# Performance work log

Measured on AMD Instinct MI355X. Metric: run time of the kernel, lower is better.

The kernel has to match this reference:

```python
import jax, jax.numpy as jnp
import numpy as np

N_NODES = 100000
N_EDGES = 6400000
HID = 32


def setup_inputs() -> dict:
    key = jax.random.key(0)
    ks = jax.random.split(key, 24)
    inp = {
        "x_G": jax.random.normal(ks[0], (N_NODES, 1), dtype=jnp.float32),
        "edge_index_G": jax.random.randint(ks[1], (2, N_EDGES), 0, N_NODES, dtype=jnp.int32),
        "x_H": jax.random.normal(ks[2], (N_NODES, 1), dtype=jnp.float32),
        "edge_index_H": jax.random.randint(ks[3], (2, N_EDGES), 0, N_NODES, dtype=jnp.int32),
    }
    ki = 4
    for i in range(3):
        d_in = 1 if i == 0 else HID
        inp[f"W1_{i}"] = jax.random.normal(ks[ki], (d_in, HID), dtype=jnp.float32) / np.sqrt(d_in); ki += 1
        inp[f"b1_{i}"] = jnp.zeros((HID,), dtype=jnp.float32)
        inp[f"W2_{i}"] = jax.random.normal(ks[ki], (HID, HID), dtype=jnp.float32) / np.sqrt(HID); ki += 1
        inp[f"b2_{i}"] = jnp.zeros((HID,), dtype=jnp.float32)
    inp["Wc1"] = jax.random.normal(ks[ki], (2 * HID, HID), dtype=jnp.float32) / np.sqrt(2 * HID); ki += 1
    inp["bc1"] = jnp.zeros((HID,), dtype=jnp.float32)
    inp["Wc2"] = jax.random.normal(ks[ki], (HID, 1), dtype=jnp.float32) / np.sqrt(HID); ki += 1
    inp["bc2"] = jnp.zeros((1,), dtype=jnp.float32)
    return inp


def _encode(x, edge_index, layers):
    n = x.shape[0]
    src, dst = edge_index[0], edge_index[1]
    for (W1, b1, W2, b2) in layers:
        # GIN aggregation: sum of neighbor messages scattered to targets; eps = 0
        agg = jax.ops.segment_sum(x[src], dst, num_segments=n)  # [N, d]
        h = x + agg  # (1 + eps) * x + agg with eps = 0
        h = jax.nn.relu(h @ W1 + b1) @ W2 + b2  # GIN MLP
        x = jax.nn.relu(h)  # outer F.relu in encode loop
    return jnp.sum(x, axis=0, keepdims=True)  # global_add_pool, single graph -> [1, HID]


def reference(x_G, edge_index_G, x_H, edge_index_H,
              W1_0, b1_0, W2_0, b2_0,
              W1_1, b1_1, W2_1, b2_1,
              W1_2, b1_2, W2_2, b2_2,
              Wc1, bc1, Wc2, bc2):
    layers = [(W1_0, b1_0, W2_0, b2_0),
              (W1_1, b1_1, W2_1, b2_1),
              (W1_2, b1_2, W2_2, b2_2)]
    h_G = _encode(x_G, edge_index_G, layers)
    h_H = _encode(x_H, edge_index_H, layers)
    combined = jnp.concatenate([h_G, h_H], axis=1)  # [1, 2*HID]
    out = jax.nn.relu(combined @ Wc1 + bc1) @ Wc2 + bc2
    return jax.nn.sigmoid(out)
```

## Files before the change

### kernel.cpp

```cpp
#include <hip/hip_runtime.h>
#include <hip/hip_bf16.h>
#include <math.h>
#include <string.h>

#define HID 32
#define PSHIFT 8
#define NPB (1 << PSHIFT)
#define MAXP 512
#define SLOTS 17408
#define SBITS 3
#define SBINS (1 << SBITS)
#define NBINS (NPB * SBINS)
#define GS 32
#define HS_ROWS 32
#define COLBUF 3072
#define COLBUF0 6144
typedef unsigned short u16;
typedef unsigned char u8;
typedef float f32x2 __attribute__((ext_vector_type(2)));

__device__ inline float e42f_sw(unsigned b) {
    unsigned u = (b & 0x7fu) << 20;
    float f; memcpy(&f, &u, 4);
    return f * 0x1p120f;
}
__device__ inline unsigned f2e4_sw(float f) {
    f = fminf(f, 448.f);
    float y = f * 0x1p-120f;
    unsigned r; memcpy(&r, &y, 4);
    r = r + 0x7FFFFu + ((r >> 20) & 1u);
    return (r >> 20) & 0x7fu;
}
__device__ inline void acc_e4(float* a, unsigned w) {
#if __has_builtin(__builtin_amdgcn_cvt_pk_f32_fp8)
    f32x2 lo = __builtin_amdgcn_cvt_pk_f32_fp8(w, false);
    f32x2 hi = __builtin_amdgcn_cvt_pk_f32_fp8(w, true);
    a[0] += lo.x; a[1] += lo.y; a[2] += hi.x; a[3] += hi.y;
#else
    a[0] += e42f_sw(w);
    a[1] += e42f_sw(w >> 8);
    a[2] += e42f_sw(w >> 16);
    a[3] += e42f_sw(w >> 24);
#endif
}
__device__ inline unsigned pack_e4(float o0, float o1, float o2, float o3) {
#if __has_builtin(__builtin_amdgcn_cvt_pk_fp8_f32)
    unsigned pw = (unsigned)__builtin_amdgcn_cvt_pk_fp8_f32(
        fminf(o0, 448.f), fminf(o1, 448.f), 0, false);
    pw = (unsigned)__builtin_amdgcn_cvt_pk_fp8_f32(
        fminf(o2, 448.f), fminf(o3, 448.f), pw, true);
    return pw;
#else
    return f2e4_sw(o0) | (f2e4_sw(o1) << 8) | (f2e4_sw(o2) << 16) | (f2e4_sw(o3) << 24);
#endif
}

__global__ void zero_kernel(float* __restrict__ p, int n) {
    int i = blockIdx.x * blockDim.x + threadIdx.x;
    if (i < n) p[i] = 0.f;
}
__global__ void init_gcur(int* __restrict__ gcur, int P) {
    int b = blockIdx.x * blockDim.x + threadIdx.x;
    if (b < P) gcur[b * GS] = b * SLOTS;
}

__global__ void partition_edges(const int* __restrict__ src, const int* __restrict__ dst,
                                int* __restrict__ gcur, unsigned* __restrict__ staged,
                                int E, int P) {
    __shared__ int h[4][MAXP];
    __shared__ int hbase[MAXP];
    __shared__ int cur[MAXP];
    __shared__ int gbase[MAXP];
    __shared__ unsigned sortedv[4096];
    __shared__ u16 bktid[4096];
    __shared__ int wsums[4];
    __shared__ int sTotal;
    int t = threadIdx.x, wid = t >> 6, lane = t & 63;
    for (int i = t; i < 4 * MAXP; i += 256) (&h[0][0])[i] = 0;
    __syncthreads();

    int base = blockIdx.x * 4096;
    int4 S[4], D[4];
#pragma unroll
    for (int r = 0; r < 4; r++) {
        int e = base + r * 1024 + t * 4;
        if (e + 3 < E) {
            S[r] = *(const int4*)(src + e);
            D[r] = *(const int4*)(dst + e);
        } else {
            int s0[4], d0[4];
            for (int j = 0; j < 4; j++) {
                int ee = e + j;
                s0[j] = (ee < E) ? src[ee] : -1;
                d0[j] = (ee < E) ? dst[ee] : -1;
            }
            S[r] = make_int4(s0[0], s0[1], s0[2], s0[3]);
            D[r] = make_int4(d0[0], d0[1], d0[2], d0[3]);
        }
        if (D[r].x >= 0) atomicAdd(&h[wid][D[r].x >> PSHIFT], 1);
        if (D[r].y >= 0) atomicAdd(&h[wid][D[r].y >> PSHIFT], 1);
        if (D[r].z >= 0) atomicAdd(&h[wid][D[r].z >> PSHIFT], 1);
        if (D[r].w >= 0) atomicAdd(&h[wid][D[r].w >> PSHIFT], 1);
    }
    __syncthreads();

    int b0 = 2 * t, b1 = 2 * t + 1;
    int t0 = (b0 < P) ? (h[0][b0] + h[1][b0] + h[2][b0] + h[3][b0]) : 0;
    int t1 = (b1 < P) ? (h[0][b1] + h[1][b1] + h[2][b1] + h[3][b1]) : 0;
    int s = t0 + t1;
    int incl = s;
#pragma unroll
    for (int off = 1; off < 64; off <<= 1) {
        int u = __shfl_up(incl, off, 64);
        if (lane >= off) incl += u;
    }
    if (lane == 63) wsums[wid] = incl;
    __syncthreads();
    int woff = 0;
#pragma unroll
    for (int w = 0; w < 4; w++) if (w < wid) woff += wsums[w];
    int excl = woff + incl - s;
    if (b0 < P) { hbase[b0] = excl;      cur[b0] = excl; }
    if (b1 < P) { hbase[b1] = excl + t0; cur[b1] = excl + t0; }
    if (b0 < P && t0) gbase[b0] = atomicAdd(&gcur[b0 * GS], t0);
    if (b1 < P && t1) gbase[b1] = atomicAdd(&gcur[b1 * GS], t1);
    if (t == 255) sTotal = excl + s;
    __syncthreads();

#pragma unroll
    for (int r = 0; r < 4; r++) {
        int ss[4] = { S[r].x, S[r].y, S[r].z, S[r].w };
        int dd[4] = { D[r].x, D[r].y, D[r].z, D[r].w };
#pragma unroll
        for (int j = 0; j < 4; j++) {
            int d = dd[j];
            if (d >= 0) {
                int bk = d >> PSHIFT;
                int pos = atomicAdd(&cur[bk], 1);
                sortedv[pos] = ((unsigned)(d & (NPB - 1)) << 17) | (unsigned)ss[j];
                bktid[pos]   = (u16)bk;
            }
        }
    }
    __syncthreads();

    int total = sTotal;
    for (int i = t; i < total; i += 256) {
        int bk = bktid[i];
        int addr = gbase[bk] + (i - hbase[bk]);
        if (addr < (bk + 1) * SLOTS)
            staged[addr] = sortedv[i];
    }
}

__global__ void scan_buckets(const int* __restrict__ gcur, int* __restrict__ colbase,
                             int* __restrict__ rowptr, int P, int N) {
    __shared__ int wsums[4];
    int t = threadIdx.x, wid = t >> 6, lane = t & 63;
    int b0 = 2 * t, b1 = 2 * t + 1;
    int c0 = 0, c1 = 0;
    if (b0 < P) { c0 = gcur[b0 * GS] - b0 * SLOTS; if (c0 > SLOTS) c0 = SLOTS; }
    if (b1 < P) { c1 = gcur[b1 * GS] - b1 * SLOTS; if (c1 > SLOTS) c1 = SLOTS; }
    int s = c0 + c1;
    int incl = s;
#pragma unroll
    for (int off = 1; off < 64; off <<= 1) {
        int u = __shfl_up(incl, off, 64);
        if (lane >= off) incl += u;
    }
    if (lane == 63) wsums[wid] = incl;
    __syncthreads();
    int woff = 0;
#pragma unroll
    for (int w = 0; w < 4; w++) if (w < wid) woff += wsums[w];
    int excl = woff + incl - s;
    if (b0 < P) colbase[b0] = excl;
    if (b1 < P) colbase[b1] = excl + c0;
    if (t == 255) {
        colbase[P] = excl + s;
        rowptr[N]  = excl + s;
    }
}

__global__ void sort_bucket(const unsigned* __restrict__ staged, const int* __restrict__ gcur,
                            const int* __restrict__ colbase,
                            int* __restrict__ rowptr, int* __restrict__ col, int N) {
    __shared__ int cnt[NBINS];
    __shared__ int wsum[4];
    __shared__ int sorted[SLOTS];
    int b = blockIdx.x;
    int t = threadIdx.x;
    int lane = t & 63, wid = t >> 6;
    int sBeg = b * SLOTS;
    int sEnd = gcur[b * GS]; if (sEnd > sBeg + SLOTS) sEnd = sBeg + SLOTS;
    int total = sEnd - sBeg;
    int colStart = colbase[b];
    int nodeBase = b << PSHIFT;

    for (int i = t; i < NBINS; i += 256) cnt[i] = 0;
    __syncthreads();
    for (int i = sBeg + t; i < sEnd; i += 256) {
        unsigned w = staged[i];
        int key = (int)((w >> 17) << SBITS) | (int)((w & 0x1FFFFu) >> 14);
        atomicAdd(&cnt[key], 1);
    }
    __syncthreads();

    int loc[SBINS]; int tot = 0;
#pragma unroll
    for (int k = 0; k < SBINS; k++) { loc[k] = tot; tot += cnt[(t << SBITS) + k]; }
    int incl = tot;
#pragma unroll
    for (int off = 1; off < 64; off <<= 1) {
        int u = __shfl_up(incl, off, 64);
        if (lane >= off) incl += u;
    }
    if (lane == 63) wsum[wid] = incl;
    __syncthreads();
    int woff = 0;
#pragma unroll
    for (int w = 0; w < 4; w++) if (w < wid) woff += wsum[w];
    int excl = woff + incl - tot;
    int node = nodeBase + t;
    if (node < N) rowptr[node] = colStart + excl;
#pragma unroll
    for (int k = 0; k < SBINS; k++) cnt[(t << SBITS) + k] = excl + loc[k];
    __syncthreads();

    for (int i = sBeg + t; i < sEnd; i += 256) {
        unsigned w = staged[i];
        int key = (int)((w >> 17) << SBITS) | (int)((w & 0x1FFFFu) >> 14);
        int pos = atomicAdd(&cnt[key], 1);
        sorted[pos] = (int)(w & 0x1FFFFu);
    }
    __syncthreads();
    for (int i = t; i < total; i += 256)
        col[colStart + i] = sorted[i];
}

__global__ void mlp0_fused(const int* __restrict__ rowptr, const int* __restrict__ col,
                           const float* __restrict__ x0,
                           const float* __restrict__ W1, const float* __restrict__ b1,
                           const float* __restrict__ W2, const float* __restrict__ b2,
                           u8* __restrict__ out, int n) {
    __shared__ float sW1[HID], sb1[HID], sW2[HID * HID], sb2[HID];
    __shared__ int colbuf[COLBUF0];
    int t = threadIdx.x;
    if (t < HID) { sW1[t] = W1[t]; sb1[t] = b1[t]; sb2[t] = b2[t]; }
    for (int i = t; i < HID * HID; i += blockDim.x) sW2[i] = W2[i];

    int firstNode = blockIdx.x * 64;
    int lastNode  = firstNode + 64; if (lastNode > n) lastNode = n;
    int blockStart = (firstNode < n) ? rowptr[firstNode] : 0;
    int blockEnd   = (firstNode < n) ? rowptr[lastNode] : 0;
    int stagedCnt = blockEnd - blockStart; if (stagedCnt > COLBUF0) stagedCnt = COLBUF0;
    for (int i = t; i < stagedCnt; i += 256) colbuf[i] = col[blockStart + i];
    __syncthreads();

    int node = firstNode + (t >> 2);
    int q    = t & 3;
    int lane = t & 63;
    int base = lane & ~3;
    bool active = node < n;

    float s = 0.f;
    if (active) {
        int beg = rowptr[node], end = rowptr[node + 1];
        int jSplit = blockStart + stagedCnt; if (jSplit > end) jSplit = end;
        int j = beg + q;
        for (; j + 12 < jSplit; j += 16) {
            int c0 = colbuf[j - blockStart];
            int c1 = colbuf[j + 4 - blockStart];
            int c2 = colbuf[j + 8 - blockStart];
            int c3 = colbuf[j + 12 - blockStart];
            s += x0[c0]; s += x0[c1]; s += x0[c2]; s += x0[c3];
        }
        for (; j < jSplit; j += 4) s += x0[colbuf[j - blockStart]];
        for (; j < end; j += 4) s += x0[col[j]];
    }
    s += __shfl_xor(s, 1, 64);
    s += __shfl_xor(s, 2, 64);
    float v = active ? (x0[node] + s) : 0.f;

    float h[8];
#pragma unroll
    for (int i = 0; i < 8; i++) h[i] = fmaxf(fmaf(v, sW1[q * 8 + i], sb1[q * 8 + i]), 0.f);
    float o[8];
#pragma unroll
    for (int i = 0; i < 8; i++) o[i] = sb2[q * 8 + i];
#pragma unroll
    for (int k = 0; k < HID; k++) {
        float hk = __shfl(h[k & 7], base | (k >> 3), 64);
#pragma unroll
        for (int i = 0; i < 8; i++) o[i] = fmaf(hk, sW2[k * HID + q * 8 + i], o[i]);
    }
    if (active) {
        unsigned w0 = pack_e4(fmaxf(o[0], 0.f), fmaxf(o[1], 0.f),
                              fmaxf(o[2], 0.f), fmaxf(o[3], 0.f));
        unsigned w1 = pack_e4(fmaxf(o[4], 0.f), fmaxf(o[5], 0.f),
                              fmaxf(o[6], 0.f), fmaxf(o[7], 0.f));
        uint2 pk = make_uint2(w0, w1);
        *(uint2*)(out + ((size_t)node << 5) + (q << 3)) = pk;
    }
}

template <bool REDUCE>
__global__ void mlp_fused(const int* __restrict__ rowptr, const int* __restrict__ col,
                          const u8* __restrict__ xin,
                          const float* __restrict__ W1, const float* __restrict__ b1,
                          const float* __restrict__ W2, const float* __restrict__ b2,
                          u8* __restrict__ xout, float* __restrict__ hsum, int n) {
    __shared__ float sW1[HID * HID], sb1[HID], sW2[HID * HID], sb2[HID];
    __shared__ int colbuf[COLBUF];
    __shared__ float red[4][HID];
    int t = threadIdx.x;
    for (int i = t; i < HID * HID; i += blockDim.x) { sW1[i] = W1[i]; sW2[i] = W2[i]; }
    if (t < HID) { sb1[t] = b1[t]; sb2[t] = b2[t]; }

    int firstNode = blockIdx.x * 32;
    int lastNode  = firstNode + 32; if (lastNode > n) lastNode = n;
    int blockStart = (firstNode < n) ? rowptr[firstNode] : 0;
    int blockEnd   = (firstNode < n) ? rowptr[lastNode] : 0;
    int stagedCnt = blockEnd - blockStart; if (stagedCnt > COLBUF) stagedCnt = COLBUF;
    for (int i = t; i < stagedCnt; i += 256) colbuf[i] = col[blockStart + i];
    __syncthreads();

    int node = firstNode + (t >> 3);
    int q    = t & 7;
    int lane = t & 63;
    int base = lane & ~7;
    bool active = node < n;

    float va[4];
#pragma unroll
    for (int i = 0; i < 4; i++) va[i] = 0.f;
    if (active) {
        int beg = rowptr[node], end = rowptr[node + 1];
        const u8* xq = xin + (q << 2);
        float a0[4], a1[4], a2[4], a3[4];
#pragma unroll
        for (int i = 0; i < 4; i++) a0[i] = a1[i] = a2[i] = a3[i] = 0.f;
        {
            unsigned w = *(const unsigned*)(xq + ((size_t)node << 5));
            acc_e4(a0, w);
        }
        int jSplit = blockStart + stagedCnt; if (jSplit > end) jSplit = end;
        int j = beg;
        for (; j + 8 <= jSplit; j += 8) {
            int lj = j - blockStart;
            int c0 = colbuf[lj+0], c1 = colbuf[lj+1], c2 = colbuf[lj+2], c3 = colbuf[lj+3];
            int c4 = colbuf[lj+4], c5 = colbuf[lj+5], c6 = colbuf[lj+6], c7 = colbuf[lj+7];
            unsigned w0 = *(const unsigned*)(xq + ((size_t)c0 << 5));
            unsigned w1 = *(const unsigned*)(xq + ((size_t)c1 << 5));
            unsigned w2 = *(const unsigned*)(xq + ((size_t)c2 << 5));
            unsigned w3 = *(const unsigned*)(xq + ((size_t)c3 << 5));
            unsigned w4 = *(const unsigned*)(xq + ((size_t)c4 << 5));
            unsigned w5 = *(const unsigned*)(xq + ((size_t)c5 << 5));
            unsigned w6 = *(const unsigned*)(xq + ((size_t)c6 << 5));
            unsigned w7 = *(const unsigned*)(xq + ((size_t)c7 << 5));
            acc_e4(a0, w0); acc_e4(a1, w1); acc_e4(a2, w2); acc_e4(a3, w3);
            acc_e4(a0, w4); acc_e4(a1, w5); acc_e4(a2, w6); acc_e4(a3, w7);
        }
        for (; j < jSplit; j++) {
            unsigned w = *(const unsigned*)(xq + ((size_t)colbuf[j - blockStart] << 5));
            acc_e4(a0, w);
        }
        for (; j < end; j++) {
            unsigned w = *(const unsigned*)(xq + ((size_t)col[j] << 5));
            acc_e4(a0, w);
        }
#pragma unroll
        for (int i = 0; i < 4; i++) va[i] = (a0[i] + a1[i]) + (a2[i] + a3[i]);
    }

    float h[4];
#pragma unroll
    for (int i = 0; i < 4; i++) h[i] = sb1[q * 4 + i];
#pragma unroll
    for (int k = 0; k < HID; k++) {
        float vk = __shfl(va[k & 3], base | (k >> 2), 64);
#pragma unroll
        for (int i = 0; i < 4; i++) h[i] = fmaf(vk, sW1[k * HID + q * 4 + i], h[i]);
    }
#pragma unroll
    for (int i = 0; i < 4; i++) h[i] = fmaxf(h[i], 0.f);

    float o[4];
#pragma unroll
    for (int i = 0; i < 4; i++) o[i] = sb2[q * 4 + i];
#pragma unroll
    for (int k = 0; k < HID; k++) {
        float hk = __shfl(h[k & 3], base | (k >> 2), 64);
#pragma unroll
        for (int i = 0; i < 4; i++) o[i] = fmaf(hk, sW2[k * HID + q * 4 + i], o[i]);
    }
#pragma unroll
    for (int i = 0; i < 4; i++) o[i] = fmaxf(o[i], 0.f);

    if (REDUCE) {
        if (!active) {
#pragma unroll
            for (int i = 0; i < 4; i++) o[i] = 0.f;
        }
#pragma unroll
        for (int i = 0; i < 4; i++) {
            float v = o[i];
            v += __shfl_xor(v, 8, 64);
            v += __shfl_xor(v, 16, 64);
            v += __shfl_xor(v, 32, 64);
            o[i] = v;
        }
        int wid = t >> 6;
        if (lane < 8) {
#pragma unroll
            for (int i = 0; i < 4; i++) red[wid][lane * 4 + i] = o[i];
        }
        __syncthreads();
        if (t < HID) {
            float s = red[0][t] + red[1][t] + red[2][t] + red[3][t];
            atomicAdd(&hsum[(blockIdx.x & (HS_ROWS - 1)) * (2 * HID) + t], s);
        }
    } else if (active) {
        unsigned pw = pack_e4(o[0], o[1], o[2], o[3]);
        *(unsigned*)(xout + ((size_t)node << 5) + (q << 2)) = pw;
    }
}

__global__ void head_kernel(const float* __restrict__ hsumP,
                            const float* __restrict__ Wc1, const float* __restrict__ bc1,
                            const float* __restrict__ Wc2, const float* __restrict__ bc2,
                            float* __restrict__ out) {
    __shared__ float hs[2 * HID];
    int t = threadIdx.x;
    if (t < 2 * HID) {
        float s = 0.f;
        for (int r = 0; r < HS_ROWS; r++) s += hsumP[r * (2 * HID) + t];
        hs[t] = s;
    }
    __syncthreads();
    float val = 0.f;
    if (t < HID) {
        float acc = bc1[t];
        for (int i = 0; i < 2 * HID; i++) acc = fmaf(hs[i], Wc1[i * HID + t], acc);
        val = fmaxf(acc, 0.f) * Wc2[t];
    }
    for (int off = 32; off >= 1; off >>= 1) val += __shfl_xor(val, off, 64);
    if (t == 0) out[0] = 1.f / (1.f + expf(-(val + bc2[0])));
}

extern "C" void kernel_launch(void* const* d_in, const int* in_sizes, int n_in,
                              void* d_out, int out_size, void* d_ws, size_t ws_size,
                              hipStream_t stream) {
    const float* xg[2] = { (const float*)d_in[0], (const float*)d_in[2] };
    const int*   eg[2] = { (const int*)d_in[1],   (const int*)d_in[3] };
    const float* W1[3] = { (const float*)d_in[4], (const float*)d_in[8],  (const float*)d_in[12] };
    const float* b1[3] = { (const float*)d_in[5], (const float*)d_in[9],  (const float*)d_in[13] };
    const float* W2[3] = { (const float*)d_in[6], (const float*)d_in[10], (const float*)d_in[14] };
    const float* b2[3] = { (const float*)d_in[7], (const float*)d_in[11], (const float*)d_in[15] };
    const float* Wc1 = (const float*)d_in[16];
    const float* bc1 = (const float*)d_in[17];
    const float* Wc2 = (const float*)d_in[18];
    const float* bc2 = (const float*)d_in[19];

    const int N = in_sizes[0];
    const int E = in_sizes[1] / 2;
    const int P = (N + NPB - 1) >> PSHIFT;

    u8*       B0      = (u8*)d_ws;
    u8*       B1      = B0 + (size_t)N * 32;
    float*    hsumP   = (float*)(B1 + (size_t)N * 32);
    int*      rowptr  = (int*)(hsumP + HS_ROWS * 2 * HID);
    int*      col     = rowptr + (N + 1);
    int*      colbase = col + (size_t)E;
    int*      gcur    = colbase + (P + 1);
    unsigned* staged  = (unsigned*)(gcur + (size_t)P * GS);

    const int TB = 256;
    dim3 blk(TB);
    int gE4k = (E + 4095) / 4096;
    int gN64 = (N + 63) / 64;
    int gN8  = (N + 31) / 32;
    int gP   = (P + TB - 1) / TB;

    zero_kernel<<<(HS_ROWS * 2 * HID + 255) / 256, 256, 0, stream>>>(hsumP, HS_ROWS * 2 * HID);

    for (int g = 0; g < 2; g++) {
        const float* x0  = xg[g];
        const int*   src = eg[g];
        const int*   dst = src + E;

        init_gcur<<<gP, blk, 0, stream>>>(gcur, P);
        partition_edges<<<gE4k, blk, 0, stream>>>(src, dst, gcur, staged, E, P);
        scan_buckets<<<1, blk, 0, stream>>>(gcur, colbase, rowptr, P, N);
        sort_bucket<<<P, blk, 0, stream>>>(staged, gcur, colbase, rowptr, col, N);

        mlp0_fused<<<gN64, blk, 0, stream>>>(rowptr, col, x0, W1[0], b1[0], W2[0], b2[0], B0, N);

        mlp_fused<false><<<gN8, blk, 0, stream>>>(rowptr, col, B0, W1[1], b1[1], W2[1], b2[1],
                                                  B1, nullptr, N);

        mlp_fused<true><<<gN8, blk, 0, stream>>>(rowptr, col, B1, W1[2], b1[2], W2[2], b2[2],
                                                 nullptr, hsumP + g * HID, N);
    }

    head_kernel<<<1, 64, 0, stream>>>(hsumP, Wc1, bc1, Wc2, bc2, (float*)d_out);
}
```

Before: 571.5 us.

## Replace bucketed two-pass CSR sort with global histogram, scan and atomic scatter

Replaces the CSR build (LDS-bucketed partition into staged slots plus per-bucket counting sort) with a plain counting sort: global atomic histogram on dst, a three-kernel prefix scan into rowptr, and an atomic-cursor scatter of src into col. This drops the staged intermediate buffer, the SLOTS overflow cap and the extra LDS sorting passes. In exchange it issues about 12.8M global atomics per graph with random addresses, and the within-row order of col becomes nondeterministic, which can change how the sum reduction rounds.

```diff
diff --git a/kernel.cpp b/kernel.cpp
--- a/kernel.cpp
+++ b/kernel.cpp
@@ -4,14 +4,6 @@
 #include <string.h>
 
 #define HID 32
-#define PSHIFT 8
-#define NPB (1 << PSHIFT)
-#define MAXP 512
-#define SLOTS 17408
-#define SBITS 3
-#define SBINS (1 << SBITS)
-#define NBINS (NPB * SBINS)
-#define GS 32
 #define HS_ROWS 32
 #define COLBUF 3072
 #define COLBUF0 6144
@@ -59,55 +51,46 @@
     int i = blockIdx.x * blockDim.x + threadIdx.x;
     if (i < n) p[i] = 0.f;
 }
-__global__ void init_gcur(int* __restrict__ gcur, int P) {
-    int b = blockIdx.x * blockDim.x + threadIdx.x;
-    if (b < P) gcur[b * GS] = b * SLOTS;
-}
-
-__global__ void partition_edges(const int* __restrict__ src, const int* __restrict__ dst,
-                                int* __restrict__ gcur, unsigned* __restrict__ staged,
-                                int E, int P) {
-    __shared__ int h[4][MAXP];
-    __shared__ int hbase[MAXP];
-    __shared__ int cur[MAXP];
-    __shared__ int gbase[MAXP];
-    __shared__ unsigned sortedv[4096];
-    __shared__ u16 bktid[4096];
+__global__ void zero_int(int* __restrict__ p, int n) {
+    int i = blockIdx.x * blockDim.x + threadIdx.x;
+    if (i < n) p[i] = 0;
+}
+
+__global__ void hist_edges(const int* __restrict__ dst, int* __restrict__ cnt, int E) {
+    int e = (blockIdx.x * blockDim.x + threadIdx.x) * 4;
+    if (e + 3 < E) {
+        int4 D = *(const int4*)(dst + e);
+        atomicAdd(&cnt[D.x], 1);
+        atomicAdd(&cnt[D.y], 1);
+        atomicAdd(&cnt[D.z], 1);
+        atomicAdd(&cnt[D.w], 1);
+    } else {
+        for (int j = e; j < E && j < e + 4; j++) atomicAdd(&cnt[dst[j]], 1);
+    }
+}
+
+__global__ void scan_partial(const int* __restrict__ cnt, int* __restrict__ bsum, int N) {
     __shared__ int wsums[4];
-    __shared__ int sTotal;
     int t = threadIdx.x, wid = t >> 6, lane = t & 63;
-    for (int i = t; i < 4 * MAXP; i += 256) (&h[0][0])[i] = 0;
-    __syncthreads();
-
-    int base = blockIdx.x * 4096;
-    int4 S[4], D[4];
-#pragma unroll
-    for (int r = 0; r < 4; r++) {
-        int e = base + r * 1024 + t * 4;
-        if (e + 3 < E) {
-            S[r] = *(const int4*)(src + e);
-            D[r] = *(const int4*)(dst + e);
-        } else {
-            int s0[4], d0[4];
-            for (int j = 0; j < 4; j++) {
-                int ee = e + j;
-                s0[j] = (ee < E) ? src[ee] : -1;
-                d0[j] = (ee < E) ? dst[ee] : -1;
-            }
-            S[r] = make_int4(s0[0], s0[1], s0[2], s0[3]);
-            D[r] = make_int4(d0[0], d0[1], d0[2], d0[3]);
-        }
-        if (D[r].x >= 0) atomicAdd(&h[wid][D[r].x >> PSHIFT], 1);
-        if (D[r].y >= 0) atomicAdd(&h[wid][D[r].y >> PSHIFT], 1);
-        if (D[r].z >= 0) atomicAdd(&h[wid][D[r].z >> PSHIFT], 1);
-        if (D[r].w >= 0) atomicAdd(&h[wid][D[r].w >> PSHIFT], 1);
-    }
-    __syncthreads();
-
-    int b0 = 2 * t, b1 = 2 * t + 1;
-    int t0 = (b0 < P) ? (h[0][b0] + h[1][b0] + h[2][b0] + h[3][b0]) : 0;
-    int t1 = (b1 < P) ? (h[0][b1] + h[1][b1] + h[2][b1] + h[3][b1]) : 0;
-    int s = t0 + t1;
+    int base = blockIdx.x * 1024 + t * 4;
+    int s = 0;
+#pragma unroll
+    for (int j = 0; j < 4; j++) { int idx = base + j; if (idx < N) s += cnt[idx]; }
+#pragma unroll
+    for (int off = 1; off < 64; off <<= 1) s += __shfl_xor(s, off, 64);
+    if (lane == 0) wsums[wid] = s;
+    __syncthreads();
+    if (t == 0) bsum[blockIdx.x] = wsums[0] + wsums[1] + wsums[2] + wsums[3];
+}
+
+__global__ void scan_blocksums(int* __restrict__ bsum, int* __restrict__ rowptr,
+                               int nb, int N) {
+    __shared__ int wsums[4];
+    int t = threadIdx.x, wid = t >> 6, lane = t & 63;
+    int b0 = 4 * t;
+    int v[4]; int s = 0;
+#pragma unroll
+    for (int j = 0; j < 4; j++) { int b = b0 + j; v[j] = (b < nb) ? bsum[b] : 0; s += v[j]; }
     int incl = s;
 #pragma unroll
     for (int off = 1; off < 64; off <<= 1) {
@@ -120,48 +103,24 @@
 #pragma unroll
     for (int w = 0; w < 4; w++) if (w < wid) woff += wsums[w];
     int excl = woff + incl - s;
-    if (b0 < P) { hbase[b0] = excl;      cur[b0] = excl; }
-    if (b1 < P) { hbase[b1] = excl + t0; cur[b1] = excl + t0; }
-    if (b0 < P && t0) gbase[b0] = atomicAdd(&gcur[b0 * GS], t0);
-    if (b1 < P && t1) gbase[b1] = atomicAdd(&gcur[b1 * GS], t1);
-    if (t == 255) sTotal = excl + s;
-    __syncthreads();
-
-#pragma unroll
-    for (int r = 0; r < 4; r++) {
-        int ss[4] = { S[r].x, S[r].y, S[r].z, S[r].w };
-        int dd[4] = { D[r].x, D[r].y, D[r].z, D[r].w };
-#pragma unroll
-        for (int j = 0; j < 4; j++) {
-            int d = dd[j];
-            if (d >= 0) {
-                int bk = d >> PSHIFT;
-                int pos = atomicAdd(&cur[bk], 1);
-                sortedv[pos] = ((unsigned)(d & (NPB - 1)) << 17) | (unsigned)ss[j];
-                bktid[pos]   = (u16)bk;
-            }
-        }
-    }
-    __syncthreads();
-
-    int total = sTotal;
-    for (int i = t; i < total; i += 256) {
-        int bk = bktid[i];
-        int addr = gbase[bk] + (i - hbase[bk]);
-        if (addr < (bk + 1) * SLOTS)
-            staged[addr] = sortedv[i];
-    }
-}
-
-__global__ void scan_buckets(const int* __restrict__ gcur, int* __restrict__ colbase,
-                             int* __restrict__ rowptr, int P, int N) {
+    int runx = excl;
+#pragma unroll
+    for (int j = 0; j < 4; j++) {
+        int b = b0 + j;
+        if (b < nb) bsum[b] = runx;
+        runx += v[j];
+    }
+    if (t == 0) rowptr[N] = wsums[0] + wsums[1] + wsums[2] + wsums[3];
+}
+
+__global__ void scan_write(const int* __restrict__ cnt, const int* __restrict__ bsum,
+                           int* __restrict__ rowptr, int* __restrict__ curp, int N) {
     __shared__ int wsums[4];
     int t = threadIdx.x, wid = t >> 6, lane = t & 63;
-    int b0 = 2 * t, b1 = 2 * t + 1;
-    int c0 = 0, c1 = 0;
-    if (b0 < P) { c0 = gcur[b0 * GS] - b0 * SLOTS; if (c0 > SLOTS) c0 = SLOTS; }
-    if (b1 < P) { c1 = gcur[b1 * GS] - b1 * SLOTS; if (c1 > SLOTS) c1 = SLOTS; }
-    int s = c0 + c1;
+    int base = blockIdx.x * 1024 + t * 4;
+    int v[4]; int s = 0;
+#pragma unroll
+    for (int j = 0; j < 4; j++) { int idx = base + j; v[j] = (idx < N) ? cnt[idx] : 0; s += v[j]; }
     int incl = s;
 #pragma unroll
     for (int off = 1; off < 64; off <<= 1) {
@@ -173,69 +132,29 @@
     int woff = 0;
 #pragma unroll
     for (int w = 0; w < 4; w++) if (w < wid) woff += wsums[w];
-    int excl = woff + incl - s;
-    if (b0 < P) colbase[b0] = excl;
-    if (b1 < P) colbase[b1] = excl + c0;
-    if (t == 255) {
-        colbase[P] = excl + s;
-        rowptr[N]  = excl + s;
-    }
-}
-
-__global__ void sort_bucket(const unsigned* __restrict__ staged, const int* __restrict__ gcur,
-                            const int* __restrict__ colbase,
-                            int* __restrict__ rowptr, int* __restrict__ col, int N) {
-    __shared__ int cnt[NBINS];
-    __shared__ int wsum[4];
-    __shared__ int sorted[SLOTS];
-    int b = blockIdx.x;
-    int t = threadIdx.x;
-    int lane = t & 63, wid = t >> 6;
-    int sBeg = b * SLOTS;
-    int sEnd = gcur[b * GS]; if (sEnd > sBeg + SLOTS) sEnd = sBeg + SLOTS;
-    int total = sEnd - sBeg;
-    int colStart = colbase[b];
-    int nodeBase = b << PSHIFT;
-
-    for (int i = t; i < NBINS; i += 256) cnt[i] = 0;
-    __syncthreads();
-    for (int i = sBeg + t; i < sEnd; i += 256) {
-        unsigned w = staged[i];
-        int key = (int)((w >> 17) << SBITS) | (int)((w & 0x1FFFFu) >> 14);
-        atomicAdd(&cnt[key], 1);
-    }
-    __syncthreads();
-
-    int loc[SBINS]; int tot = 0;
-#pragma unroll
-    for (int k = 0; k < SBINS; k++) { loc[k] = tot; tot += cnt[(t << SBITS) + k]; }
-    int incl = tot;
-#pragma unroll
-    for (int off = 1; off < 64; off <<= 1) {
-        int u = __shfl_up(incl, off, 64);
-        if (lane >= off) incl += u;
-    }
-    if (lane == 63) wsum[wid] = incl;
-    __syncthreads();
-    int woff = 0;
-#pragma unroll
-    for (int w = 0; w < 4; w++) if (w < wid) woff += wsum[w];
-    int excl = woff + incl - tot;
-    int node = nodeBase + t;
-    if (node < N) rowptr[node] = colStart + excl;
-#pragma unroll
-    for (int k = 0; k < SBINS; k++) cnt[(t << SBITS) + k] = excl + loc[k];
-    __syncthreads();
-
-    for (int i = sBeg + t; i < sEnd; i += 256) {
-        unsigned w = staged[i];
-        int key = (int)((w >> 17) << SBITS) | (int)((w & 0x1FFFFu) >> 14);
-        int pos = atomicAdd(&cnt[key], 1);
-        sorted[pos] = (int)(w & 0x1FFFFu);
-    }
-    __syncthreads();
-    for (int i = t; i < total; i += 256)
-        col[colStart + i] = sorted[i];
+    int excl = woff + incl - s + bsum[blockIdx.x];
+    int runx = excl;
+#pragma unroll
+    for (int j = 0; j < 4; j++) {
+        int idx = base + j;
+        if (idx < N) { rowptr[idx] = runx; curp[idx] = runx; runx += v[j]; }
+    }
+}
+
+__global__ void scatter_edges(const int* __restrict__ src, const int* __restrict__ dst,
+                              int* __restrict__ curp, int* __restrict__ col, int E) {
+    int e = (blockIdx.x * blockDim.x + threadIdx.x) * 4;
+    if (e + 3 < E) {
+        int4 S = *(const int4*)(src + e);
+        int4 D = *(const int4*)(dst + e);
+        col[atomicAdd(&curp[D.x], 1)] = S.x;
+        col[atomicAdd(&curp[D.y], 1)] = S.y;
+        col[atomicAdd(&curp[D.z], 1)] = S.z;
+        col[atomicAdd(&curp[D.w], 1)] = S.w;
+    } else {
+        for (int j = e; j < E && j < e + 4; j++)
+            col[atomicAdd(&curp[dst[j]], 1)] = src[j];
+    }
 }
 
 __global__ void mlp0_fused(const int* __restrict__ rowptr, const int* __restrict__ col,
@@ -464,23 +383,23 @@
 
     const int N = in_sizes[0];
     const int E = in_sizes[1] / 2;
-    const int P = (N + NPB - 1) >> PSHIFT;
 
     u8*       B0      = (u8*)d_ws;
     u8*       B1      = B0 + (size_t)N * 32;
     float*    hsumP   = (float*)(B1 + (size_t)N * 32);
     int*      rowptr  = (int*)(hsumP + HS_ROWS * 2 * HID);
     int*      col     = rowptr + (N + 1);
-    int*      colbase = col + (size_t)E;
-    int*      gcur    = colbase + (P + 1);
-    unsigned* staged  = (unsigned*)(gcur + (size_t)P * GS);
+    int*      cnt     = col + (size_t)E;
+    int*      curp    = cnt + N;
+    int*      bsum    = curp + N;
 
     const int TB = 256;
     dim3 blk(TB);
-    int gE4k = (E + 4095) / 4096;
+    int gE4  = (E / 4 + TB - 1) / TB;
+    int nb   = (N + 1023) / 1024;
     int gN64 = (N + 63) / 64;
     int gN8  = (N + 31) / 32;
-    int gP   = (P + TB - 1) / TB;
+    int gNz  = (N + TB - 1) / TB;
 
     zero_kernel<<<(HS_ROWS * 2 * HID + 255) / 256, 256, 0, stream>>>(hsumP, HS_ROWS * 2 * HID);
 
@@ -489,10 +408,12 @@
         const int*   src = eg[g];
         const int*   dst = src + E;
 
-        init_gcur<<<gP, blk, 0, stream>>>(gcur, P);
-        partition_edges<<<gE4k, blk, 0, stream>>>(src, dst, gcur, staged, E, P);
-        scan_buckets<<<1, blk, 0, stream>>>(gcur, colbase, rowptr, P, N);
-        sort_bucket<<<P, blk, 0, stream>>>(staged, gcur, colbase, rowptr, col, N);
+        zero_int<<<gNz, blk, 0, stream>>>(cnt, N);
+        hist_edges<<<gE4, blk, 0, stream>>>(dst, cnt, E);
+        scan_partial<<<nb, blk, 0, stream>>>(cnt, bsum, N);
+        scan_blocksums<<<1, blk, 0, stream>>>(bsum, rowptr, nb, N);
+        scan_write<<<nb, blk, 0, stream>>>(cnt, bsum, rowptr, curp, N);
+        scatter_edges<<<gE4, blk, 0, stream>>>(src, dst, curp, col, E);
 
         mlp0_fused<<<gN64, blk, 0, stream>>>(rowptr, col, x0, W1[0], b1[0], W2[0], b2[0], B0, N);
 
```

Result: slower. 1.706 ms (+198.5%).

## Batch both graphs into single launches and simplify bucket sort

Applied to the files above, without the earlier changes.

Each stage now processes graphs G and H in one launch, selecting per-graph buffers by block index, which halves the launch count and doubles the grid so the GPU stays fuller. Separate workspace copies are allocated when space allows, with a sequential fallback otherwise. The sort_bucket kernel drops the sub-bin sort and LDS staging buffer, scattering column indices directly to global memory with one counter per node. Within-row neighbor order becomes nondeterministic, which is harmless for a sum, but the global scatter writes are less coalesced.

```diff
diff --git a/kernel.cpp b/kernel.cpp
--- a/kernel.cpp
+++ b/kernel.cpp
@@ -8,9 +8,6 @@
 #define NPB (1 << PSHIFT)
 #define MAXP 512
 #define SLOTS 17408
-#define SBITS 3
-#define SBINS (1 << SBITS)
-#define NBINS (NPB * SBINS)
 #define GS 32
 #define HS_ROWS 32
 #define COLBUF 3072
@@ -59,14 +56,17 @@
     int i = blockIdx.x * blockDim.x + threadIdx.x;
     if (i < n) p[i] = 0.f;
 }
-__global__ void init_gcur(int* __restrict__ gcur, int P) {
-    int b = blockIdx.x * blockDim.x + threadIdx.x;
-    if (b < P) gcur[b * GS] = b * SLOTS;
-}
-
-__global__ void partition_edges(const int* __restrict__ src, const int* __restrict__ dst,
-                                int* __restrict__ gcur, unsigned* __restrict__ staged,
-                                int E, int P) {
+__global__ void init_gcur2(int* __restrict__ gA, int* __restrict__ gB, int P) {
+    int i = blockIdx.x * blockDim.x + threadIdx.x;
+    if (i < P) gA[i * GS] = i * SLOTS;
+    else if (i < 2 * P) { int b = i - P; gB[b * GS] = b * SLOTS; }
+}
+
+__global__ void partition_edges(const int* __restrict__ srcA, const int* __restrict__ dstA,
+                                int* __restrict__ gcurA, unsigned* __restrict__ stagedA,
+                                const int* __restrict__ srcB, const int* __restrict__ dstB,
+                                int* __restrict__ gcurB, unsigned* __restrict__ stagedB,
+                                int gsplit, int E, int P) {
     __shared__ int h[4][MAXP];
     __shared__ int hbase[MAXP];
     __shared__ int cur[MAXP];
@@ -75,11 +75,16 @@
     __shared__ u16 bktid[4096];
     __shared__ int wsums[4];
     __shared__ int sTotal;
+    const int* src; const int* dst; int* gcur; unsigned* staged;
+    int bid = blockIdx.x;
+    if (bid < gsplit) { src = srcA; dst = dstA; gcur = gcurA; staged = stagedA; }
+    else { bid -= gsplit; src = srcB; dst = dstB; gcur = gcurB; staged = stagedB; }
+
     int t = threadIdx.x, wid = t >> 6, lane = t & 63;
     for (int i = t; i < 4 * MAXP; i += 256) (&h[0][0])[i] = 0;
     __syncthreads();
 
-    int base = blockIdx.x * 4096;
+    int base = bid * 4096;
     int4 S[4], D[4];
 #pragma unroll
     for (int r = 0; r < 4; r++) {
@@ -153,9 +158,14 @@
     }
 }
 
-__global__ void scan_buckets(const int* __restrict__ gcur, int* __restrict__ colbase,
-                             int* __restrict__ rowptr, int P, int N) {
+__global__ void scan_buckets(const int* __restrict__ gcurA, int* __restrict__ colbaseA,
+                             int* __restrict__ rowptrA,
+                             const int* __restrict__ gcurB, int* __restrict__ colbaseB,
+                             int* __restrict__ rowptrB, int P, int N) {
     __shared__ int wsums[4];
+    const int* gcur; int* colbase; int* rowptr;
+    if (blockIdx.x == 0) { gcur = gcurA; colbase = colbaseA; rowptr = rowptrA; }
+    else { gcur = gcurB; colbase = colbaseB; rowptr = rowptrB; }
     int t = threadIdx.x, wid = t >> 6, lane = t & 63;
     int b0 = 2 * t, b1 = 2 * t + 1;
     int c0 = 0, c1 = 0;
@@ -182,34 +192,33 @@
     }
 }
 
-__global__ void sort_bucket(const unsigned* __restrict__ staged, const int* __restrict__ gcur,
-                            const int* __restrict__ colbase,
-                            int* __restrict__ rowptr, int* __restrict__ col, int N) {
-    __shared__ int cnt[NBINS];
+__global__ void sort_bucket(const unsigned* __restrict__ stagedA, const int* __restrict__ gcurA,
+                            const int* __restrict__ colbaseA, int* __restrict__ rowptrA,
+                            int* __restrict__ colA,
+                            const unsigned* __restrict__ stagedB, const int* __restrict__ gcurB,
+                            const int* __restrict__ colbaseB, int* __restrict__ rowptrB,
+                            int* __restrict__ colB,
+                            int gsplit, int N) {
+    __shared__ int cnt[NPB];
     __shared__ int wsum[4];
-    __shared__ int sorted[SLOTS];
+    const unsigned* staged; const int* gcur; const int* colbase; int* rowptr; int* col;
     int b = blockIdx.x;
-    int t = threadIdx.x;
-    int lane = t & 63, wid = t >> 6;
+    if (b < gsplit) { staged = stagedA; gcur = gcurA; colbase = colbaseA; rowptr = rowptrA; col = colA; }
+    else { b -= gsplit; staged = stagedB; gcur = gcurB; colbase = colbaseB; rowptr = rowptrB; col = colB; }
+    int t = threadIdx.x, lane = t & 63, wid = t >> 6;
     int sBeg = b * SLOTS;
     int sEnd = gcur[b * GS]; if (sEnd > sBeg + SLOTS) sEnd = sBeg + SLOTS;
-    int total = sEnd - sBeg;
     int colStart = colbase[b];
     int nodeBase = b << PSHIFT;
 
-    for (int i = t; i < NBINS; i += 256) cnt[i] = 0;
-    __syncthreads();
-    for (int i = sBeg + t; i < sEnd; i += 256) {
-        unsigned w = staged[i];
-        int key = (int)((w >> 17) << SBITS) | (int)((w & 0x1FFFFu) >> 14);
-        atomicAdd(&cnt[key], 1);
-    }
-    __syncthreads();
-
-    int loc[SBINS]; int tot = 0;
-#pragma unroll
-    for (int k = 0; k < SBINS; k++) { loc[k] = tot; tot += cnt[(t << SBITS) + k]; }
-    int incl = tot;
+    cnt[t] = 0;
+    __syncthreads();
+    for (int i = sBeg + t; i < sEnd; i += 256)
+        atomicAdd(&cnt[staged[i] >> 17], 1);
+    __syncthreads();
+
+    int myc = cnt[t];
+    int incl = myc;
 #pragma unroll
     for (int off = 1; off < 64; off <<= 1) {
         int u = __shfl_up(incl, off, 64);
@@ -220,36 +229,38 @@
     int woff = 0;
 #pragma unroll
     for (int w = 0; w < 4; w++) if (w < wid) woff += wsum[w];
-    int excl = woff + incl - tot;
+    int excl = woff + incl - myc;
     int node = nodeBase + t;
     if (node < N) rowptr[node] = colStart + excl;
-#pragma unroll
-    for (int k = 0; k < SBINS; k++) cnt[(t << SBITS) + k] = excl + loc[k];
+    __syncthreads();
+    cnt[t] = colStart + excl;
     __syncthreads();
 
     for (int i = sBeg + t; i < sEnd; i += 256) {
         unsigned w = staged[i];
-        int key = (int)((w >> 17) << SBITS) | (int)((w & 0x1FFFFu) >> 14);
-        int pos = atomicAdd(&cnt[key], 1);
-        sorted[pos] = (int)(w & 0x1FFFFu);
-    }
-    __syncthreads();
-    for (int i = t; i < total; i += 256)
-        col[colStart + i] = sorted[i];
-}
-
-__global__ void mlp0_fused(const int* __restrict__ rowptr, const int* __restrict__ col,
-                           const float* __restrict__ x0,
+        int pos = atomicAdd(&cnt[w >> 17], 1);
+        col[pos] = (int)(w & 0x1FFFFu);
+    }
+}
+
+__global__ void mlp0_fused(const int* __restrict__ rowptrA, const int* __restrict__ colA,
+                           const float* __restrict__ x0A, u8* __restrict__ outA,
+                           const int* __restrict__ rowptrB, const int* __restrict__ colB,
+                           const float* __restrict__ x0B, u8* __restrict__ outB,
                            const float* __restrict__ W1, const float* __restrict__ b1,
                            const float* __restrict__ W2, const float* __restrict__ b2,
-                           u8* __restrict__ out, int n) {
+                           int gsplit, int n) {
     __shared__ float sW1[HID], sb1[HID], sW2[HID * HID], sb2[HID];
     __shared__ int colbuf[COLBUF0];
+    const int* rowptr; const int* col; const float* x0; u8* out;
+    int bid = blockIdx.x;
+    if (bid < gsplit) { rowptr = rowptrA; col = colA; x0 = x0A; out = outA; }
+    else { bid -= gsplit; rowptr = rowptrB; col = colB; x0 = x0B; out = outB; }
     int t = threadIdx.x;
     if (t < HID) { sW1[t] = W1[t]; sb1[t] = b1[t]; sb2[t] = b2[t]; }
     for (int i = t; i < HID * HID; i += blockDim.x) sW2[i] = W2[i];
 
-    int firstNode = blockIdx.x * 64;
+    int firstNode = bid * 64;
     int lastNode  = firstNode + 64; if (lastNode > n) lastNode = n;
     int blockStart = (firstNode < n) ? rowptr[firstNode] : 0;
     int blockEnd   = (firstNode < n) ? rowptr[lastNode] : 0;
@@ -305,19 +316,27 @@
 }
 
 template <bool REDUCE>
-__global__ void mlp_fused(const int* __restrict__ rowptr, const int* __restrict__ col,
-                          const u8* __restrict__ xin,
+__global__ void mlp_fused(const int* __restrict__ rowptrA, const int* __restrict__ colA,
+                          const u8* __restrict__ xinA, u8* __restrict__ xoutA,
+                          float* __restrict__ hsumA,
+                          const int* __restrict__ rowptrB, const int* __restrict__ colB,
+                          const u8* __restrict__ xinB, u8* __restrict__ xoutB,
+                          float* __restrict__ hsumB,
                           const float* __restrict__ W1, const float* __restrict__ b1,
                           const float* __restrict__ W2, const float* __restrict__ b2,
-                          u8* __restrict__ xout, float* __restrict__ hsum, int n) {
+                          int gsplit, int n) {
     __shared__ float sW1[HID * HID], sb1[HID], sW2[HID * HID], sb2[HID];
     __shared__ int colbuf[COLBUF];
     __shared__ float red[4][HID];
+    const int* rowptr; const int* col; const u8* xin; u8* xout; float* hsum;
+    int bid = blockIdx.x;
+    if (bid < gsplit) { rowptr = rowptrA; col = colA; xin = xinA; xout = xoutA; hsum = hsumA; }
+    else { bid -= gsplit; rowptr = rowptrB; col = colB; xin = xinB; xout = xoutB; hsum = hsumB; }
     int t = threadIdx.x;
     for (int i = t; i < HID * HID; i += blockDim.x) { sW1[i] = W1[i]; sW2[i] = W2[i]; }
     if (t < HID) { sb1[t] = b1[t]; sb2[t] = b2[t]; }
 
-    int firstNode = blockIdx.x * 32;
+    int firstNode = bid * 32;
     int lastNode  = firstNode + 32; if (lastNode > n) lastNode = n;
     int blockStart = (firstNode < n) ? rowptr[firstNode] : 0;
     int blockEnd   = (firstNode < n) ? rowptr[lastNode] : 0;
@@ -466,42 +485,83 @@
     const int E = in_sizes[1] / 2;
     const int P = (N + NPB - 1) >> PSHIFT;
 
-    u8*       B0      = (u8*)d_ws;
-    u8*       B1      = B0 + (size_t)N * 32;
-    float*    hsumP   = (float*)(B1 + (size_t)N * 32);
-    int*      rowptr  = (int*)(hsumP + HS_ROWS * 2 * HID);
-    int*      col     = rowptr + (N + 1);
-    int*      colbase = col + (size_t)E;
-    int*      gcur    = colbase + (P + 1);
-    unsigned* staged  = (unsigned*)(gcur + (size_t)P * GS);
-
     const int TB = 256;
     dim3 blk(TB);
     int gE4k = (E + 4095) / 4096;
     int gN64 = (N + 63) / 64;
     int gN8  = (N + 31) / 32;
-    int gP   = (P + TB - 1) / TB;
-
-    zero_kernel<<<(HS_ROWS * 2 * HID + 255) / 256, 256, 0, stream>>>(hsumP, HS_ROWS * 2 * HID);
-
-    for (int g = 0; g < 2; g++) {
-        const float* x0  = xg[g];
-        const int*   src = eg[g];
-        const int*   dst = src + E;
-
-        init_gcur<<<gP, blk, 0, stream>>>(gcur, P);
-        partition_edges<<<gE4k, blk, 0, stream>>>(src, dst, gcur, staged, E, P);
-        scan_buckets<<<1, blk, 0, stream>>>(gcur, colbase, rowptr, P, N);
-        sort_bucket<<<P, blk, 0, stream>>>(staged, gcur, colbase, rowptr, col, N);
-
-        mlp0_fused<<<gN64, blk, 0, stream>>>(rowptr, col, x0, W1[0], b1[0], W2[0], b2[0], B0, N);
-
-        mlp_fused<false><<<gN8, blk, 0, stream>>>(rowptr, col, B0, W1[1], b1[1], W2[1], b2[1],
-                                                  B1, nullptr, N);
-
-        mlp_fused<true><<<gN8, blk, 0, stream>>>(rowptr, col, B1, W1[2], b1[2], W2[2], b2[2],
-                                                 nullptr, hsumP + g * HID, N);
-    }
-
-    head_kernel<<<1, 64, 0, stream>>>(hsumP, Wc1, bc1, Wc2, bc2, (float*)d_out);
-}
+
+    size_t szB    = (size_t)N * 32;
+    size_t szRow  = (size_t)(N + 1) * 4;
+    size_t szCol  = (size_t)E * 4;
+    size_t szCb   = (size_t)(P + 1) * 4;
+    size_t szGcur = (size_t)P * GS * 4;
+    size_t szStg  = (size_t)P * SLOTS * 4;
+    size_t szHsum = (size_t)HS_ROWS * 2 * HID * 4;
+    size_t needBatched = 4 * szB + szHsum + 2 * (szRow + szCol + szCb + szGcur + szStg) + 1024;
+
+    char* w = (char*)d_ws;
+    auto take = [&](size_t sz) { char* p = w; w += (sz + 255) & ~(size_t)255; return p; };
+
+    if (ws_size >= needBatched) {
+        u8*    B0[2]  = { (u8*)take(szB), (u8*)take(szB) };
+        u8*    B1[2]  = { (u8*)take(szB), (u8*)take(szB) };
+        float* hsumP  = (float*)take(szHsum);
+        int*   rowp[2] = { (int*)take(szRow), (int*)take(szRow) };
+        int*   col[2]  = { (int*)take(szCol), (int*)take(szCol) };
+        int*   cb[2]   = { (int*)take(szCb), (int*)take(szCb) };
+        int*   gc[2]   = { (int*)take(szGcur), (int*)take(szGcur) };
+        unsigned* st[2] = { (unsigned*)take(szStg), (unsigned*)take(szStg) };
+
+        zero_kernel<<<(HS_ROWS * 2 * HID + 255) / 256, 256, 0, stream>>>(hsumP, HS_ROWS * 2 * HID);
+        init_gcur2<<<(2 * P + TB - 1) / TB, blk, 0, stream>>>(gc[0], gc[1], P);
+        partition_edges<<<2 * gE4k, blk, 0, stream>>>(eg[0], eg[0] + E, gc[0], st[0],
+                                                      eg[1], eg[1] + E, gc[1], st[1],
+                                                      gE4k, E, P);
+        scan_buckets<<<2, blk, 0, stream>>>(gc[0], cb[0], rowp[0], gc[1], cb[1], rowp[1], P, N);
+        sort_bucket<<<2 * P, blk, 0, stream>>>(st[0], gc[0], cb[0], rowp[0], col[0],
+                                               st[1], gc[1], cb[1], rowp[1], col[1], P, N);
+        mlp0_fused<<<2 * gN64, blk, 0, stream>>>(rowp[0], col[0], xg[0], B0[0],
+                                                 rowp[1], col[1], xg[1], B0[1],
+                                                 W1[0], b1[0], W2[0], b2[0], gN64, N);
+        mlp_fused<false><<<2 * gN8, blk, 0, stream>>>(rowp[0], col[0], B0[0], B1[0], nullptr,
+                                                      rowp[1], col[1], B0[1], B1[1], nullptr,
+                                                      W1[1], b1[1], W2[1], b2[1], gN8, N);
+        mlp_fused<true><<<2 * gN8, blk, 0, stream>>>(rowp[0], col[0], B1[0], nullptr, hsumP,
+                                                     rowp[1], col[1], B1[1], nullptr, hsumP + HID,
+                                                     W1[2], b1[2], W2[2], b2[2], gN8, N);
+        head_kernel<<<1, 64, 0, stream>>>(hsumP, Wc1, bc1, Wc2, bc2, (float*)d_out);
+    } else {
+        u8*    B0s    = (u8*)take(szB);
+        u8*    B1s    = (u8*)take(szB);
+        float* hsumP  = (float*)take(szHsum);
+        int*   rowp   = (int*)take(szRow);
+        int*   colp   = (int*)take(szCol);
+        int*   cbp    = (int*)take(szCb);
+        int*   gcp    = (int*)take(szGcur);
+        unsigned* stp = (unsigned*)take(szStg);
+
+        zero_kernel<<<(HS_ROWS * 2 * HID + 255) / 256, 256, 0, stream>>>(hsumP, HS_ROWS * 2 * HID);
+        for (int g = 0; g < 2; g++) {
+            const float* x0  = xg[g];
+            const int*   src = eg[g];
+            const int*   dst = src + E;
+            init_gcur2<<<(P + TB - 1) / TB, blk, 0, stream>>>(gcp, gcp, P);
+            partition_edges<<<gE4k, blk, 0, stream>>>(src, dst, gcp, stp,
+                                                      src, dst, gcp, stp, gE4k, E, P);
+            scan_buckets<<<1, blk, 0, stream>>>(gcp, cbp, rowp, gcp, cbp, rowp, P, N);
+            sort_bucket<<<P, blk, 0, stream>>>(stp, gcp, cbp, rowp, colp,
+                                               stp, gcp, cbp, rowp, colp, P, N);
+            mlp0_fused<<<gN64, blk, 0, stream>>>(rowp, colp, x0, B0s,
+                                                 rowp, colp, x0, B0s,
+                                                 W1[0], b1[0], W2[0], b2[0], gN64, N);
+            mlp_fused<false><<<gN8, blk, 0, stream>>>(rowp, colp, B0s, B1s, nullptr,
+                                                      rowp, colp, B0s, B1s, nullptr,
+                                                      W1[1], b1[1], W2[1], b2[1], gN8, N);
+            mlp_fused<true><<<gN8, blk, 0, stream>>>(rowp, colp, B1s, nullptr, hsumP + g * HID,
+                                                     rowp, colp, B1s, nullptr, hsumP + g * HID,
+                                                     W1[2], b1[2], W2[2], b2[2], gN8, N);
+        }
+        head_kernel<<<1, 64, 0, stream>>>(hsumP, Wc1, bc1, Wc2, bc2, (float*)d_out);
+    }
+}
```

After: 567.1 us. No clear change (-0.8%).
